# Performance work log

Measured on AMD Instinct MI355X. Metric: run time of the kernel, lower is better.

Reference implementation:

```python
import jax, jax.numpy as jnp
import numpy as np

N_NODES = 100000
N_EDGES = 3200000
IN_C, HID, OUT_C = 128, 256, 128
N_GRAPHS = 64
EPS = 1e-5


def setup_inputs() -> dict:
    key = jax.random.key(0)
    ks = jax.random.split(key, 16)
    x = jax.random.normal(ks[0], (N_NODES, IN_C), dtype=jnp.float32)
    edge_index = jax.random.randint(ks[1], (2, N_EDGES), 0, N_NODES, dtype=jnp.int64 if jax.config.jax_enable_x64 else jnp.int32)
    batch = jnp.sort(jax.random.randint(ks[2], (N_NODES,), 0, N_GRAPHS, dtype=jnp.int32))
    def glorot(k, shape):
        lim = jnp.sqrt(6.0 / (shape[-2] + shape[-1]))
        return jax.random.uniform(k, shape, jnp.float32, -lim, lim)
    return {
        "x": x,
        "W_in": glorot(ks[3], (IN_C, HID)),
        "b_in": jnp.zeros((HID,), jnp.float32),
        "g_in": jnp.ones((HID,), jnp.float32),
        "be_in": jnp.zeros((HID,), jnp.float32),
        "W_hid": glorot(ks[4], (2, HID, HID)),
        "b_hid": jnp.zeros((2, HID), jnp.float32),
        "g_hid": jnp.ones((2, HID), jnp.float32),
        "be_hid": jnp.zeros((2, HID), jnp.float32),
        "W_out": glorot(ks[5], (HID, OUT_C)),
        "b_out": jnp.zeros((OUT_C,), jnp.float32),
        "g_out": jnp.ones((OUT_C,), jnp.float32),
        "be_out": jnp.zeros((OUT_C,), jnp.float32),
        "edge_index": edge_index,
        "batch": batch,
    }


def _gcn_norm(edge_index, n_nodes):
    # add self-loops, symmetric deg^-1/2 normalization (PyG GCNConv defaults)
    loop = jnp.arange(n_nodes, dtype=edge_index.dtype)
    src = jnp.concatenate([edge_index[0], loop])
    dst = jnp.concatenate([edge_index[1], loop])
    deg = jax.ops.segment_sum(jnp.ones_like(dst, dtype=jnp.float32), dst, num_segments=n_nodes)
    dinv = jnp.where(deg > 0, jax.lax.rsqrt(deg), 0.0)
    norm = dinv[src] * dinv[dst]  # [E+N]
    return src, dst, norm


def _block(x, W, b, g, be, src, dst, norm, n_nodes):
    h = x @ W  # [N, out]
    agg = jax.ops.segment_sum(h[src] * norm[:, None], dst, num_segments=n_nodes) + b
    a = jax.nn.leaky_relu(agg, negative_slope=0.01)
    mu = jnp.mean(a, axis=0)
    var = jnp.mean(jnp.square(a - mu), axis=0)
    return (a - mu) * jax.lax.rsqrt(var + EPS) * g + be


def reference(x, W_in, b_in, g_in, be_in, W_hid, b_hid, g_hid, be_hid,
              W_out, b_out, g_out, be_out, edge_index, batch):
    n = x.shape[0]
    src, dst, norm = _gcn_norm(edge_index, n)
    h = _block(x, W_in, b_in, g_in, be_in, src, dst, norm, n)
    for i in range(W_hid.shape[0]):
        h = _block(h, W_hid[i], b_hid[i], g_hid[i], be_hid[i], src, dst, norm, n)
    h = _block(h, W_out, b_out, g_out, be_out, src, dst, norm, n)
    # global mean pool over graphs
    sums = jax.ops.segment_sum(h, batch, num_segments=N_GRAPHS)
    cnts = jax.ops.segment_sum(jnp.ones((n,), h.dtype), batch, num_segments=N_GRAPHS)
    return sums / jnp.maximum(cnts, 1.0)[:, None]
```

## Files before the change

kernel.cpp:

```cpp
#include <hip/hip_runtime.h>
#include <stdint.h>

#define EPS_LN 1e-5f

typedef short bf16x8 __attribute__((ext_vector_type(8)));
typedef float f32x4  __attribute__((ext_vector_type(4)));

__device__ __forceinline__ unsigned short f2bf(float f) {
    unsigned u = __float_as_uint(f);
    unsigned r = (u + 0x7fffu + ((u >> 16) & 1u)) >> 16;
    return (unsigned short)r;
}
__device__ __forceinline__ float bf_lo(unsigned u) { return __uint_as_float(u << 16); }
__device__ __forceinline__ float bf_hi(unsigned u) { return __uint_as_float(u & 0xffff0000u); }

__device__ __forceinline__ void async16(void* lds, const void* g) {
    __builtin_amdgcn_global_load_lds(
        (const __attribute__((address_space(1))) unsigned int*)g,
        (__attribute__((address_space(3))) unsigned int*)lds, 16, 0, 0);
}

__global__ void setup_kernel(const int* __restrict__ dst, int E,
                             unsigned* __restrict__ deg, unsigned* __restrict__ rank,
                             const float* __restrict__ x, unsigned* __restrict__ xbf, int n2,
                             const float* __restrict__ W_in, unsigned short* __restrict__ Wt_in,
                             const float* __restrict__ W_hid, unsigned short* __restrict__ Wt_h0,
                             unsigned short* __restrict__ Wt_h1) {
    int i = blockIdx.x * blockDim.x + threadIdx.x;
    if (i < E) {
        rank[i] = atomicAdd(&deg[dst[i]], 1u);
        return;
    }
    int j = i - E;
    if (j < n2) {
        float2 v = *reinterpret_cast<const float2*>(&x[(size_t)j * 2]);
        xbf[j] = (unsigned)f2bf(v.x) | ((unsigned)f2bf(v.y) << 16);
        return;
    }
    int r = j - n2;
    if (r < 32768) {
        int k = r >> 8, c = r & 255;
        Wt_in[(size_t)c * 128 + k] = f2bf(W_in[r]);
    } else if (r < 32768 + 65536) {
        r -= 32768;
        int k = r >> 8, c = r & 255;
        Wt_h0[(size_t)c * 256 + k] = f2bf(W_hid[r]);
    } else if (r < 32768 + 131072) {
        r -= 32768 + 65536;
        int k = r >> 8, c = r & 255;
        Wt_h1[(size_t)c * 256 + k] = f2bf(W_hid[65536 + r]);
    }
}

__global__ void block_sums_kernel(const unsigned* __restrict__ deg, unsigned* __restrict__ part, int N) {
    __shared__ unsigned s[256];
    int t = threadIdx.x;
    int i0 = blockIdx.x * 512 + t * 2;
    unsigned a = (i0 < N) ? deg[i0] : 0u;
    unsigned b = (i0 + 1 < N) ? deg[i0 + 1] : 0u;
    s[t] = a + b;
    __syncthreads();
    for (int off = 128; off > 0; off >>= 1) {
        if (t < off) s[t] += s[t + off];
        __syncthreads();
    }
    if (t == 0) part[blockIdx.x] = s[0];
}

__global__ void scan_part_kernel(unsigned* __restrict__ part, unsigned* __restrict__ row_ptr,
                                 int NB, int N) {
    __shared__ unsigned s[256];
    int t = threadIdx.x;
    unsigned v = (t < NB) ? part[t] : 0u;
    s[t] = v;
    __syncthreads();
    for (int off = 1; off < 256; off <<= 1) {
        unsigned u = (t >= off) ? s[t - off] : 0u;
        __syncthreads();
        s[t] += u;
        __syncthreads();
    }
    if (t < NB) part[t] = s[t] - v;
    if (t == 255) row_ptr[N] = s[255];
}

__global__ void scan_blocks_kernel(const unsigned* __restrict__ deg, const unsigned* __restrict__ part,
                                   unsigned* __restrict__ row_ptr, float* __restrict__ dinv, int N) {
    __shared__ unsigned s[256];
    int t = threadIdx.x;
    int i0 = blockIdx.x * 512 + t * 2;
    unsigned a = (i0 < N) ? deg[i0] : 0u;
    unsigned b = (i0 + 1 < N) ? deg[i0 + 1] : 0u;
    unsigned pair = a + b;
    s[t] = pair;
    __syncthreads();
    for (int off = 1; off < 256; off <<= 1) {
        unsigned u = (t >= off) ? s[t - off] : 0u;
        __syncthreads();
        s[t] += u;
        __syncthreads();
    }
    unsigned excl = s[t] - pair + part[blockIdx.x];
    if (i0 < N) {
        row_ptr[i0] = excl;
        dinv[i0] = rsqrtf((float)(a + 1u));
    }
    if (i0 + 1 < N) {
        row_ptr[i0 + 1] = excl + a;
        dinv[i0 + 1] = rsqrtf((float)(b + 1u));
    }
}

__global__ void fill_csr_kernel(const int* __restrict__ src, const int* __restrict__ dst,
                                const unsigned* __restrict__ rank, const unsigned* __restrict__ row_ptr,
                                const float* __restrict__ dinv, int E, unsigned* __restrict__ csr) {
    int e = blockIdx.x * blockDim.x + threadIdx.x;
    if (e < E) {
        int d = dst[e];
        int s = src[e];
        unsigned pos = row_ptr[d] + rank[e];
        unsigned wq = __float2uint_rn(dinv[s] * 32767.f);
        csr[pos] = (wq << 17) | (unsigned)s;
    }
}

template<int UPL, bool AFF, bool FINAL>
__global__ void aggregate_bf(const unsigned* __restrict__ X, unsigned* __restrict__ outp,
                             const unsigned* __restrict__ row_ptr, const unsigned* __restrict__ csr,
                             const float* __restrict__ dinv,
                             const float* __restrict__ ssum, const float* __restrict__ ssq,
                             const float* __restrict__ gg, const float* __restrict__ be, float invN,
                             const float* __restrict__ tW, const float* __restrict__ bias, int N) {
    constexpr int C = UPL * 64;
    constexpr unsigned RSU = C / 2;
    constexpr int PC = UPL * 2;

    __shared__ float sL[AFF ? C : 1], tL[AFF ? C : 1];
    if constexpr (AFF) {
        for (int i = threadIdx.x; i < C; i += 256) {
            float mu = ssum[i] * invN;
            float var = ssq[i] * invN - mu * mu;
            float s = gg[i] * rsqrtf(var + EPS_LN);
            sL[i] = s;
            tL[i] = be[i] - mu * s;
        }
        __syncthreads();
    }

    int node = blockIdx.x * 8 + (threadIdx.x >> 5);
    if (node >= N) return;
    int ll = threadIdx.x & 31;
    unsigned cu = (unsigned)ll * UPL;

    float di = dinv[node];
    float dscale = di * (1.f / 32767.f);
    float w0 = di * di;
    float acc[PC];
    float wsum = w0;
    {
        const unsigned* xr = X + (size_t)((unsigned)node * RSU + cu);
        if constexpr (UPL == 4) {
            uint4 v = *reinterpret_cast<const uint4*>(xr);
            unsigned uu[4] = {v.x, v.y, v.z, v.w};
            #pragma unroll
            for (int q = 0; q < 4; ++q) {
                acc[q * 2 + 0] = w0 * bf_lo(uu[q]);
                acc[q * 2 + 1] = w0 * bf_hi(uu[q]);
            }
        } else {
            uint2 v = *reinterpret_cast<const uint2*>(xr);
            acc[0] = w0 * bf_lo(v.x); acc[1] = w0 * bf_hi(v.x);
            acc[2] = w0 * bf_lo(v.y); acc[3] = w0 * bf_hi(v.y);
        }
    }
    unsigned e0 = row_ptr[node];
    unsigned e1 = row_ptr[node + 1];
    unsigned cnt = e1 - e0;
    unsigned full = cnt & ~7u;

    for (unsigned i = 0; i < full; i += 8) {
        unsigned p[8];
        #pragma unroll
        for (int u = 0; u < 8; ++u) p[u] = csr[e0 + i + u];
        if constexpr (UPL == 4) {
            uint4 v[8];
            #pragma unroll
            for (int u = 0; u < 8; ++u)
                v[u] = *reinterpret_cast<const uint4*>(X + (size_t)((p[u] & 0x1FFFFu) * RSU + cu));
            #pragma unroll
            for (int u = 0; u < 8; ++u) {
                float f = (float)(p[u] >> 17) * dscale;
                unsigned uu[4] = {v[u].x, v[u].y, v[u].z, v[u].w};
                #pragma unroll
                for (int q = 0; q < 4; ++q) {
                    acc[q * 2 + 0] += f * bf_lo(uu[q]);
                    acc[q * 2 + 1] += f * bf_hi(uu[q]);
                }
                wsum += f;
            }
        } else {
            uint2 v[8];
            #pragma unroll
            for (int u = 0; u < 8; ++u)
                v[u] = *reinterpret_cast<const uint2*>(X + (size_t)((p[u] & 0x1FFFFu) * RSU + cu));
            #pragma unroll
            for (int u = 0; u < 8; ++u) {
                float f = (float)(p[u] >> 17) * dscale;
                acc[0] += f * bf_lo(v[u].x); acc[1] += f * bf_hi(v[u].x);
                acc[2] += f * bf_lo(v[u].y); acc[3] += f * bf_hi(v[u].y);
                wsum += f;
            }
        }
    }
    for (unsigned i = full; i < cnt; ++i) {
        unsigned p = csr[e0 + i];
        float f = (float)(p >> 17) * dscale;
        if constexpr (UPL == 4) {
            uint4 v = *reinterpret_cast<const uint4*>(X + (size_t)((p & 0x1FFFFu) * RSU + cu));
            unsigned uu[4] = {v.x, v.y, v.z, v.w};
            #pragma unroll
            for (int q = 0; q < 4; ++q) {
                acc[q * 2 + 0] += f * bf_lo(uu[q]);
                acc[q * 2 + 1] += f * bf_hi(uu[q]);
            }
        } else {
            uint2 v = *reinterpret_cast<const uint2*>(X + (size_t)((p & 0x1FFFFu) * RSU + cu));
            acc[0] += f * bf_lo(v.x); acc[1] += f * bf_hi(v.x);
            acc[2] += f * bf_lo(v.y); acc[3] += f * bf_hi(v.y);
        }
        wsum += f;
    }

    int col = ll * PC;
    float z[PC];
    #pragma unroll
    for (int j = 0; j < PC; ++j) {
        float f = acc[j];
        if constexpr (AFF) f = sL[col + j] * f + tL[col + j] * wsum;
        if constexpr (FINAL) {
            f = f + wsum * tW[col + j] + bias[col + j];
            f = f > 0.f ? f : 0.01f * f;
        }
        z[j] = f;
    }
    if constexpr (UPL == 4) {
        uint4 pk;
        pk.x = (unsigned)f2bf(z[0]) | ((unsigned)f2bf(z[1]) << 16);
        pk.y = (unsigned)f2bf(z[2]) | ((unsigned)f2bf(z[3]) << 16);
        pk.z = (unsigned)f2bf(z[4]) | ((unsigned)f2bf(z[5]) << 16);
        pk.w = (unsigned)f2bf(z[6]) | ((unsigned)f2bf(z[7]) << 16);
        *reinterpret_cast<uint4*>(&outp[(size_t)((unsigned)node * RSU + cu)]) = pk;
    } else {
        uint2 pk;
        pk.x = (unsigned)f2bf(z[0]) | ((unsigned)f2bf(z[1]) << 16);
        pk.y = (unsigned)f2bf(z[2]) | ((unsigned)f2bf(z[3]) << 16);
        *reinterpret_cast<uint2*>(&outp[(size_t)((unsigned)node * RSU + cu)]) = pk;
    }
}

template<int K, int NN, bool EPI>
__launch_bounds__(256)
__global__ void gemm_mfma(const unsigned short* __restrict__ Z, const unsigned short* __restrict__ Wt,
                          const float* __restrict__ bias, unsigned short* __restrict__ out,
                          float* __restrict__ stat_sum, float* __restrict__ stat_sq, int M) {
    __shared__ char smem[32768];
    __shared__ float csum[128], csq[128];

    const int tid = threadIdx.x;
    const int lane = tid & 63;
    const int w = tid >> 6;
    const int wr = (w >> 1) * 64;
    const int wc = (w & 1) * 64;
    const int rowBase = blockIdx.x * 128;
    const int colBase = blockIdx.y * 128;
    const int frow = lane & 15;
    const int kgrp = lane >> 4;

    f32x4 acc[4][4] = {};

    for (int kt = 0; kt < K / 64; ++kt) {
        #pragma unroll
        for (int i = 0; i < 4; ++i) {
            int g = (i * 4 + w) * 64 + lane;
            int r = g >> 3;
            int bl = (g & 7) * 16;
            int bg = bl ^ ((r & 7) << 4);
            const char* src = (const char*)Z + (((size_t)(rowBase + r) * K + kt * 64) << 1) + bg;
            async16(&smem[(i * 4 + w) * 1024], src);
        }
        #pragma unroll
        for (int i = 0; i < 4; ++i) {
            int g = (i * 4 + w) * 64 + lane;
            int r = g >> 3;
            int bl = (g & 7) * 16;
            int bg = bl ^ ((r & 7) << 4);
            const char* src = (const char*)Wt + (((size_t)(colBase + r) * K + kt * 64) << 1) + bg;
            async16(&smem[16384 + (i * 4 + w) * 1024], src);
        }
        __syncthreads();
        #pragma unroll
        for (int kk = 0; kk < 2; ++kk) {
            const int kbyte = kk * 64 + kgrp * 16;
            bf16x8 af[4], bfr[4];
            #pragma unroll
            for (int m = 0; m < 4; ++m) {
                int r = wr + m * 16 + frow;
                af[m] = *reinterpret_cast<const bf16x8*>(&smem[r * 128 + (kbyte ^ ((r & 7) << 4))]);
            }
            #pragma unroll
            for (int n = 0; n < 4; ++n) {
                int c = wc + n * 16 + frow;
                bfr[n] = *reinterpret_cast<const bf16x8*>(&smem[16384 + c * 128 + (kbyte ^ ((c & 7) << 4))]);
            }
            #pragma unroll
            for (int m = 0; m < 4; ++m)
                #pragma unroll
                for (int n = 0; n < 4; ++n)
                    acc[m][n] = __builtin_amdgcn_mfma_f32_16x16x32_bf16(bfr[n], af[m], acc[m][n], 0, 0, 0);
        }
        __syncthreads();
    }

    if constexpr (EPI) {
        if (tid < 128) { csum[tid] = 0.f; csq[tid] = 0.f; }
        __syncthreads();
    }

    #pragma unroll
    for (int n = 0; n < 4; ++n) {
        const int c_local = wc + n * 16 + kgrp * 4;
        const int col = colBase + c_local;
        float4 b4 = make_float4(0.f, 0.f, 0.f, 0.f);
        if constexpr (EPI) b4 = *reinterpret_cast<const float4*>(&bias[col]);
        float ps[4] = {0.f, 0.f, 0.f, 0.f}, pq[4] = {0.f, 0.f, 0.f, 0.f};
        #pragma unroll
        for (int m = 0; m < 4; ++m) {
            int row = rowBase + wr + m * 16 + frow;
            if (row < M) {
                float f0 = acc[m][n][0] + b4.x;
                float f1 = acc[m][n][1] + b4.y;
                float f2 = acc[m][n][2] + b4.z;
                float f3 = acc[m][n][3] + b4.w;
                if constexpr (EPI) {
                    f0 = f0 > 0.f ? f0 : 0.01f * f0;
                    f1 = f1 > 0.f ? f1 : 0.01f * f1;
                    f2 = f2 > 0.f ? f2 : 0.01f * f2;
                    f3 = f3 > 0.f ? f3 : 0.01f * f3;
                }
                uint2 pk;
                pk.x = (unsigned)f2bf(f0) | ((unsigned)f2bf(f1) << 16);
                pk.y = (unsigned)f2bf(f2) | ((unsigned)f2bf(f3) << 16);
                *reinterpret_cast<uint2*>(&out[(size_t)row * NN + col]) = pk;
                if constexpr (EPI) {
                    ps[0] += f0; ps[1] += f1; ps[2] += f2; ps[3] += f3;
                    pq[0] += f0 * f0; pq[1] += f1 * f1; pq[2] += f2 * f2; pq[3] += f3 * f3;
                }
            }
        }
        if constexpr (EPI) {
            #pragma unroll
            for (int s = 1; s < 16; s <<= 1) {
                #pragma unroll
                for (int j = 0; j < 4; ++j) {
                    ps[j] += __shfl_xor(ps[j], s);
                    pq[j] += __shfl_xor(pq[j], s);
                }
            }
            if (frow == 0) {
                #pragma unroll
                for (int j = 0; j < 4; ++j) {
                    atomicAdd(&csum[c_local + j], ps[j]);
                    atomicAdd(&csq[c_local + j], pq[j]);
                }
            }
        }
    }
    if constexpr (EPI) {
        __syncthreads();
        if (tid < 128) {
            atomicAdd(&stat_sum[colBase + tid], csum[tid]);
            atomicAdd(&stat_sq[colBase + tid], csq[tid]);
        }
    }
}

__global__ void prep_wout_tw(const float* __restrict__ W,
                             const float* __restrict__ ssum, const float* __restrict__ ssq,
                             const float* __restrict__ gg, const float* __restrict__ be, float invN,
                             unsigned short* __restrict__ Wt, float* __restrict__ tW) {
    if (blockIdx.x < 128) {
        int idx = blockIdx.x * 256 + threadIdx.x;
        int k = idx >> 7, c = idx & 127;
        float mu = ssum[k] * invN;
        float var = ssq[k] * invN - mu * mu;
        float s = gg[k] * rsqrtf(var + EPS_LN);
        Wt[(size_t)c * 256 + k] = f2bf(s * W[idx]);
    } else {
        int c = threadIdx.x;
        if (c < 128) {
            float acc = 0.f;
            for (int k = 0; k < 256; ++k) {
                float mu = ssum[k] * invN;
                float var = ssq[k] * invN - mu * mu;
                float s = gg[k] * rsqrtf(var + EPS_LN);
                float t = be[k] - mu * s;
                acc += t * W[k * 128 + c];
            }
            tW[c] = acc;
        }
    }
}

__global__ void stats_pool_kernel(const unsigned short* __restrict__ A, const int* __restrict__ batch,
                                  float* __restrict__ stat_sum, float* __restrict__ stat_sq,
                                  float* __restrict__ psums, float* __restrict__ pcnt, int N) {
    int c = threadIdx.x;
    int n0 = blockIdx.x * 256;
    if (n0 >= N) return;
    int n1 = min(n0 + 256, N);
    float cs = 0.f, cq = 0.f;
    float acc = 0.f, cacc = 0.f;
    int curg = -1;
    for (int n = n0; n < n1; ++n) {
        float v = __uint_as_float((unsigned)A[(size_t)n * 128 + c] << 16);
        cs += v; cq += v * v;
        int g = batch[n];
        if (g != curg) {
            if (curg >= 0) {
                atomicAdd(&psums[curg * 128 + c], acc);
                if (c == 0) atomicAdd(&pcnt[curg], cacc);
            }
            acc = 0.f; cacc = 0.f; curg = g;
        }
        acc += v;
        cacc += 1.f;
    }
    if (curg >= 0) {
        atomicAdd(&psums[curg * 128 + c], acc);
        if (c == 0) atomicAdd(&pcnt[curg], cacc);
    }
    atomicAdd(&stat_sum[c], cs);
    atomicAdd(&stat_sq[c], cq);
}

__global__ void divide_kernel(const float* __restrict__ psums, const float* __restrict__ pcnt,
                              const float* __restrict__ ssum, const float* __restrict__ ssq,
                              const float* __restrict__ gg, const float* __restrict__ be, float invN,
                              float* __restrict__ out) {
    int i = blockIdx.x * blockDim.x + threadIdx.x;
    if (i < 64 * 128) {
        int g = i >> 7, c = i & 127;
        float mu = ssum[c] * invN;
        float var = ssq[c] * invN - mu * mu;
        float s = gg[c] * rsqrtf(var + EPS_LN);
        float t = be[c] - mu * s;
        float cnt = pcnt[g];
        out[i] = (cnt > 0.f) ? s * (psums[i] / cnt) + t : 0.f;
    }
}

extern "C" void kernel_launch(void* const* d_in, const int* in_sizes, int n_in,
                              void* d_out, int out_size, void* d_ws, size_t ws_size,
                              hipStream_t stream) {
    const float* x      = (const float*)d_in[0];
    const float* W_in   = (const float*)d_in[1];
    const float* b_in   = (const float*)d_in[2];
    const float* g_in   = (const float*)d_in[3];
    const float* be_in  = (const float*)d_in[4];
    const float* W_hid  = (const float*)d_in[5];
    const float* b_hid  = (const float*)d_in[6];
    const float* g_hid  = (const float*)d_in[7];
    const float* be_hid = (const float*)d_in[8];
    const float* W_out  = (const float*)d_in[9];
    const float* b_out  = (const float*)d_in[10];
    const float* g_out  = (const float*)d_in[11];
    const float* be_out = (const float*)d_in[12];
    const int*   eidx   = (const int*)d_in[13];
    const int*   batch  = (const int*)d_in[14];
    float* out = (float*)d_out;

    const int N = in_sizes[14];
    const int E = in_sizes[13] / 2;
    const int Npad = ((N + 127) / 128) * 128;
    const int NB = (N + 511) / 512;
    const int* e_src = eidx;
    const int* e_dst = eidx + E;

    char* ws = (char*)d_ws;
    size_t off = 0;
    auto alloc = [&](size_t bytes) -> void* {
        void* p = ws + off;
        off = (off + bytes + 255) & ~(size_t)255;
        return p;
    };
    char* B1 = (char*)alloc((size_t)Npad * 256 * 2);
    char* B2 = (char*)alloc((size_t)Npad * 256 * 2);
    unsigned* deg      = (unsigned*)alloc((size_t)N * 4);
    float*    dinv     = (float*)alloc((size_t)N * 4);
    unsigned* row_ptr  = (unsigned*)alloc((size_t)(N + 1) * 4);
    unsigned* rank     = (unsigned*)alloc((size_t)E * 4);
    unsigned* part     = (unsigned*)alloc(256 * 4);
    unsigned* csr      = (unsigned*)alloc((size_t)E * 4);
    unsigned short* Wt_in  = (unsigned short*)alloc(256 * 128 * 2);
    unsigned short* Wt_h0  = (unsigned short*)alloc(256 * 256 * 2);
    unsigned short* Wt_h1  = (unsigned short*)alloc(256 * 256 * 2);
    unsigned short* Wt_out = (unsigned short*)alloc(128 * 256 * 2);
    float*    tW       = (float*)alloc(128 * 4);
    float*    stats    = (float*)alloc(4 * 512 * 4);
    float*    psums    = (float*)alloc(64 * 128 * 4);
    float*    pcnt     = (float*)alloc(64 * 4);

    float* s1 = stats + 0 * 512, *q1 = s1 + 256;
    float* s2 = stats + 1 * 512, *q2 = s2 + 256;
    float* s3 = stats + 2 * 512, *q3 = s3 + 256;
    float* s4 = stats + 3 * 512, *q4 = s4 + 256;

    const float invN = 1.0f / (float)N;

    hipMemsetAsync(deg, 0, (size_t)N * 4, stream);
    hipMemsetAsync(stats, 0, ((char*)pcnt + 64 * 4) - (char*)stats, stream);

    {
        int total = E + N * 64 + 32768 + 65536 + 65536;
        setup_kernel<<<(total + 255) / 256, 256, 0, stream>>>(
            e_dst, E, deg, rank, x, (unsigned*)B2, N * 64, W_in, Wt_in, W_hid, Wt_h0, Wt_h1);
    }
    block_sums_kernel<<<NB, 256, 0, stream>>>(deg, part, N);
    scan_part_kernel<<<1, 256, 0, stream>>>(part, row_ptr, NB, N);
    scan_blocks_kernel<<<NB, 256, 0, stream>>>(deg, part, row_ptr, dinv, N);
    fill_csr_kernel<<<(E + 255) / 256, 256, 0, stream>>>(e_src, e_dst, rank, row_ptr, dinv, E, csr);

    const int aggGrid = (N + 7) / 8;
    dim3 gg256(Npad / 128, 2);

    aggregate_bf<2, false, false><<<aggGrid, 256, 0, stream>>>(
        (const unsigned*)B2, (unsigned*)B1, row_ptr, csr, dinv,
        nullptr, nullptr, nullptr, nullptr, invN, nullptr, nullptr, N);
    gemm_mfma<128, 256, true><<<gg256, 256, 0, stream>>>(
        (const unsigned short*)B1, Wt_in, b_in, (unsigned short*)B2, s1, q1, N);

    aggregate_bf<4, true, false><<<aggGrid, 256, 0, stream>>>(
        (const unsigned*)B2, (unsigned*)B1, row_ptr, csr, dinv,
        s1, q1, g_in, be_in, invN, nullptr, nullptr, N);
    gemm_mfma<256, 256, true><<<gg256, 256, 0, stream>>>(
        (const unsigned short*)B1, Wt_h0, b_hid, (unsigned short*)B2, s2, q2, N);

    aggregate_bf<4, true, false><<<aggGrid, 256, 0, stream>>>(
        (const unsigned*)B2, (unsigned*)B1, row_ptr, csr, dinv,
        s2, q2, g_hid, be_hid, invN, nullptr, nullptr, N);
    gemm_mfma<256, 256, true><<<gg256, 256, 0, stream>>>(
        (const unsigned short*)B1, Wt_h1, b_hid + 256, (unsigned short*)B2, s3, q3, N);

    prep_wout_tw<<<129, 256, 0, stream>>>(W_out, s3, q3, g_hid + 256, be_hid + 256, invN, Wt_out, tW);
    gemm_mfma<256, 128, false><<<dim3(Npad / 128, 1), 256, 0, stream>>>(
        (const unsigned short*)B2, Wt_out, nullptr, (unsigned short*)B1, nullptr, nullptr, N);
    aggregate_bf<2, false, true><<<aggGrid, 256, 0, stream>>>(
        (const unsigned*)B1, (unsigned*)B2, row_ptr, csr, dinv,
        nullptr, nullptr, nullptr, nullptr, invN, tW, b_out, N);

    stats_pool_kernel<<<(N + 255) / 256, 128, 0, stream>>>(
        (const unsigned short*)B2, batch, s4, q4, psums, pcnt, N);
    divide_kernel<<<(64 * 128 + 255) / 256, 256, 0, stream>>>(
        psums, pcnt, s4, q4, g_out, be_out, invN, out);
}
```

Before: 1.154 ms.

## Add nontemporal hints and read GEMM weights directly from global memory

Marks several streaming loads and stores (rank, CSR indices, aggregate outputs, GEMM outputs) as nontemporal to reduce cache pollution. The GEMM also stops staging the weight tile in LDS: each lane loads its B fragments straight from global memory, and the LDS buffer is halved. This removes LDS traffic for weights and may raise occupancy, but it adds uncached-pattern global loads inside the inner loop. Nontemporal stores on outputs that the next kernel reads right away could also hurt L2 reuse.

After: 1.358 ms. 1.18x slower.

```diff
diff --git a/kernel.cpp b/kernel.cpp
--- a/kernel.cpp
+++ b/kernel.cpp
@@ -5,6 +5,8 @@
 
 typedef short bf16x8 __attribute__((ext_vector_type(8)));
 typedef float f32x4  __attribute__((ext_vector_type(4)));
+typedef unsigned uint2_nt __attribute__((ext_vector_type(2)));
+typedef unsigned uint4_nt __attribute__((ext_vector_type(4)));
 
 __device__ __forceinline__ unsigned short f2bf(float f) {
     unsigned u = __float_as_uint(f);
@@ -28,7 +30,8 @@
                              unsigned short* __restrict__ Wt_h1) {
     int i = blockIdx.x * blockDim.x + threadIdx.x;
     if (i < E) {
-        rank[i] = atomicAdd(&deg[dst[i]], 1u);
+        unsigned r = atomicAdd(&deg[dst[i]], 1u);
+        __builtin_nontemporal_store(r, &rank[i]);
         return;
     }
     int j = i - E;
@@ -118,7 +121,7 @@
     if (e < E) {
         int d = dst[e];
         int s = src[e];
-        unsigned pos = row_ptr[d] + rank[e];
+        unsigned pos = row_ptr[d] + __builtin_nontemporal_load(&rank[e]);
         unsigned wq = __float2uint_rn(dinv[s] * 32767.f);
         csr[pos] = (wq << 17) | (unsigned)s;
     }
@@ -181,7 +184,7 @@
     for (unsigned i = 0; i < full; i += 8) {
         unsigned p[8];
         #pragma unroll
-        for (int u = 0; u < 8; ++u) p[u] = csr[e0 + i + u];
+        for (int u = 0; u < 8; ++u) p[u] = __builtin_nontemporal_load(&csr[e0 + i + u]);
         if constexpr (UPL == 4) {
             uint4 v[8];
             #pragma unroll
@@ -244,17 +247,17 @@
         z[j] = f;
     }
     if constexpr (UPL == 4) {
-        uint4 pk;
+        uint4_nt pk;
         pk.x = (unsigned)f2bf(z[0]) | ((unsigned)f2bf(z[1]) << 16);
         pk.y = (unsigned)f2bf(z[2]) | ((unsigned)f2bf(z[3]) << 16);
         pk.z = (unsigned)f2bf(z[4]) | ((unsigned)f2bf(z[5]) << 16);
         pk.w = (unsigned)f2bf(z[6]) | ((unsigned)f2bf(z[7]) << 16);
-        *reinterpret_cast<uint4*>(&outp[(size_t)((unsigned)node * RSU + cu)]) = pk;
+        __builtin_nontemporal_store(pk, reinterpret_cast<uint4_nt*>(&outp[(size_t)((unsigned)node * RSU + cu)]));
     } else {
-        uint2 pk;
+        uint2_nt pk;
         pk.x = (unsigned)f2bf(z[0]) | ((unsigned)f2bf(z[1]) << 16);
         pk.y = (unsigned)f2bf(z[2]) | ((unsigned)f2bf(z[3]) << 16);
-        *reinterpret_cast<uint2*>(&outp[(size_t)((unsigned)node * RSU + cu)]) = pk;
+        __builtin_nontemporal_store(pk, reinterpret_cast<uint2_nt*>(&outp[(size_t)((unsigned)node * RSU + cu)]));
     }
 }
 
@@ -263,7 +266,7 @@
 __global__ void gemm_mfma(const unsigned short* __restrict__ Z, const unsigned short* __restrict__ Wt,
                           const float* __restrict__ bias, unsigned short* __restrict__ out,
                           float* __restrict__ stat_sum, float* __restrict__ stat_sq, int M) {
-    __shared__ char smem[32768];
+    __shared__ char smem[16384];
     __shared__ float csum[128], csq[128];
 
     const int tid = threadIdx.x;
@@ -288,19 +291,11 @@
             const char* src = (const char*)Z + (((size_t)(rowBase + r) * K + kt * 64) << 1) + bg;
             async16(&smem[(i * 4 + w) * 1024], src);
         }
-        #pragma unroll
-        for (int i = 0; i < 4; ++i) {
-            int g = (i * 4 + w) * 64 + lane;
-            int r = g >> 3;
-            int bl = (g & 7) * 16;
-            int bg = bl ^ ((r & 7) << 4);
-            const char* src = (const char*)Wt + (((size_t)(colBase + r) * K + kt * 64) << 1) + bg;
-            async16(&smem[16384 + (i * 4 + w) * 1024], src);
-        }
         __syncthreads();
         #pragma unroll
         for (int kk = 0; kk < 2; ++kk) {
             const int kbyte = kk * 64 + kgrp * 16;
+            const int koff = kt * 64 + kk * 32 + kgrp * 8;
             bf16x8 af[4], bfr[4];
             #pragma unroll
             for (int m = 0; m < 4; ++m) {
@@ -309,8 +304,8 @@
             }
             #pragma unroll
             for (int n = 0; n < 4; ++n) {
-                int c = wc + n * 16 + frow;
-                bfr[n] = *reinterpret_cast<const bf16x8*>(&smem[16384 + c * 128 + (kbyte ^ ((c & 7) << 4))]);
+                int c = colBase + wc + n * 16 + frow;
+                bfr[n] = *reinterpret_cast<const bf16x8*>(Wt + (size_t)c * K + koff);
             }
             #pragma unroll
             for (int m = 0; m < 4; ++m)
@@ -347,10 +342,10 @@
                     f2 = f2 > 0.f ? f2 : 0.01f * f2;
                     f3 = f3 > 0.f ? f3 : 0.01f * f3;
                 }
-                uint2 pk;
+                uint2_nt pk;
                 pk.x = (unsigned)f2bf(f0) | ((unsigned)f2bf(f1) << 16);
                 pk.y = (unsigned)f2bf(f2) | ((unsigned)f2bf(f3) << 16);
-                *reinterpret_cast<uint2*>(&out[(size_t)row * NN + col]) = pk;
+                __builtin_nontemporal_store(pk, reinterpret_cast<uint2_nt*>(&out[(size_t)row * NN + col]));
                 if constexpr (EPI) {
                     ps[0] += f0; ps[1] += f1; ps[2] += f2; ps[3] += f3;
                     pq[0] += f0 * f0; pq[1] += f1 * f1; pq[2] += f2 * f2; pq[3] += f3 * f3;
```
